# Optimization experiments

Hardware: AMD Instinct MI355X
Metric: run time of the kernel (lower is better)

Reference implementation:

```python
import jax, jax.numpy as jnp
import numpy as np
from itertools import product as iter_product

N_QUBITS = 6
DIM = 2 ** N_QUBITS            # 64
N_GEN = DIM * DIM - 1          # 4095
DEPTH = 4
N_OBS = 15

_GENS = None

def _build_generators(n):
    I = np.eye(2, dtype=np.complex64)
    X = np.array([[0, 1], [1, 0]], np.complex64)
    Y = np.array([[0, -1j], [1j, 0]], np.complex64)
    Z = np.array([[1, 0], [0, -1]], np.complex64)
    P = [I, X, Y, Z]
    gens = []
    for idx in iter_product(range(4), repeat=n):
        if all(i == 0 for i in idx):
            continue
        m = P[idx[0]]
        for k in range(1, n):
            m = np.kron(m, P[idx[k]])
        gens.append(m)
    return jnp.asarray(np.stack(gens))  # [4^n-1, 2^n, 2^n] complex64

def _gens():
    global _GENS
    if _GENS is None:
        _GENS = _build_generators(N_QUBITS)
    return _GENS

def _apply_ry(psi, q, theta, n):
    # psi: [B, 2^n] complex; RY(theta) on qubit q
    B = psi.shape[0]
    x = psi.reshape(B, 2 ** q, 2, 2 ** (n - q - 1))
    c = jnp.cos(theta / 2)
    s = jnp.sin(theta / 2)
    s0, s1 = x[:, :, 0, :], x[:, :, 1, :]
    x = jnp.stack([c * s0 - s * s1, s * s0 + c * s1], axis=2)
    return x.reshape(B, -1)

def _apply_cnot(psi, c, t, n):
    # psi: [B, 2^n]; CNOT control c, target t
    B = psi.shape[0]
    x = psi.reshape((B,) + (2,) * n)
    ax_c, ax_t = 1 + c, 1 + t
    x0 = jnp.take(x, 0, axis=ax_c)
    x1 = jnp.take(x, 1, axis=ax_c)
    ax_t2 = ax_t - (1 if ax_t > ax_c else 0)
    x1 = jnp.flip(x1, axis=ax_t2)
    x = jnp.stack([x0, x1], axis=ax_c)
    return x.reshape(B, -1)

def _make_hermitians(A, B, D):
    # create_Hermitian vectorized over the m observables.
    # h[i,j] = A[idx]+iB[idx] for j<i (row-major lower-tri), h[i-1,i-1]=D[i];
    # then H = h + h^H.
    il, jl = jnp.tril_indices(DIM, -1)  # row-major order matches count+j loop
    di = jnp.arange(DIM - 1)

    def one(a, b, d):
        h = jnp.zeros((DIM, DIM), jnp.complex64)
        h = h.at[il, jl].set(a + 1j * b)
        h = h.at[di, di].set(d[1:].astype(jnp.complex64))
        return h + h.conj().T

    return jax.vmap(one)(A, B, D)  # [m, DIM, DIM]

def setup_inputs() -> dict:
    key = jax.random.key(0)
    ks = jax.random.split(key, 8)
    batch, input_dim, hidden = 256, 1024, 2047
    n_off = DIM * (DIM - 1) // 2  # 2016
    return {
        "x": jax.random.normal(ks[0], (batch, input_dim), jnp.float32),
        "W1": 0.02 * jax.random.normal(ks[1], (input_dim, hidden), jnp.float32),
        "b1": jnp.zeros((hidden,), jnp.float32),
        "W2": 0.02 * jax.random.normal(ks[2], (hidden, N_GEN), jnp.float32),
        "b2": jnp.zeros((N_GEN,), jnp.float32),
        "var_params": 0.01 * jax.random.normal(ks[3], (DEPTH, N_QUBITS), jnp.float32),
        "A": 2.0 * jax.random.normal(ks[4], (N_OBS, n_off), jnp.float32),
        "B": 2.0 * jax.random.normal(ks[5], (N_OBS, n_off), jnp.float32),
        "D": 2.0 * jax.random.normal(ks[6], (N_OBS, DIM), jnp.float32),
    }

def reference(x, W1, b1, W2, b2, var_params, A, B, D):
    n = N_QUBITS
    # encoding projection: Linear -> SiLU -> Linear
    h = jax.nn.silu(x @ W1 + b1)
    theta = h @ W2 + b2  # [batch, 4^n - 1]
    gens = _gens()  # [n_gen, dim, dim] complex64 (constant)
    # A_mat = sum_g theta_g G_g (Hermitian), U = exp(i A_mat)
    Amat = jnp.einsum('bg,gij->bij', theta.astype(jnp.complex64), gens)
    U = jax.vmap(jax.scipy.linalg.expm)(1j * Amat)  # [batch, dim, dim]
    psi = U[:, :, 0]  # apply to |0...0>
    # hardware-efficient VQC: RY layer + CNOT ring per depth
    for d in range(DEPTH):
        for q in range(n):
            psi = _apply_ry(psi, q, var_params[d, q], n)
        for q in range(n):
            psi = _apply_cnot(psi, q, (q + 1) % n, n)
    H = _make_hermitians(A, B, D)  # [m, dim, dim]
    # expectation <psi|H_w|psi>
    exp = jnp.einsum('bi,wij,bj->bw', psi.conj(), H, psi).real
    return exp  # [batch, n_observables]
```

## Files before the change

### kernel.cpp

```cpp
#include <hip/hip_runtime.h>
#include <math.h>

typedef unsigned short ushort_t;
typedef __attribute__((ext_vector_type(8))) short bf16x8_t;
typedef __attribute__((ext_vector_type(4))) float f32x4_t;

__device__ __forceinline__ ushort_t f2bf(float x) {
  unsigned u = __float_as_uint(x);
  unsigned r = (u + 0x7fffu + ((u >> 16) & 1u)) >> 16;
  return (ushort_t)r;
}
__device__ __forceinline__ float bf2f(ushort_t h) {
  return __uint_as_float(((unsigned)h) << 16);
}
__device__ __forceinline__ void tsplit(float v, unsigned& h, unsigned& l) {
  unsigned u = __float_as_uint(v);
  h = u >> 16;
  float lo = v - __uint_as_float(u & 0xffff0000u);
  l = __float_as_uint(lo) >> 16;
}

__device__ __forceinline__ void transpose_tile(
    const float* __restrict__ W, ushort_t* __restrict__ Wh,
    ushort_t* __restrict__ Wl, int K, int N, int Kpad, int n0, int k0, int t) {
  __shared__ float sh[32][33];
  const int tx = t & 31, ty = t >> 5;
#pragma unroll
  for (int i = 0; i < 4; ++i) {
    int k = k0 + i * 8 + ty;
    float v = (k < K && (n0 + tx) < N) ? W[(size_t)k * N + n0 + tx] : 0.f;
    sh[tx][i * 8 + ty] = v;
  }
  __syncthreads();
#pragma unroll
  for (int i = 0; i < 4; ++i) {
    int n = n0 + i * 8 + ty;
    int kk = k0 + tx;
    float v = sh[i * 8 + ty][tx];
    size_t o = (size_t)n * Kpad + kk;
    unsigned h, l;
    tsplit(v, h, l);
    Wh[o] = (ushort_t)h;
    Wl[o] = (ushort_t)l;
  }
}

__global__ __launch_bounds__(256) void prep_kernel(
    const float* __restrict__ x, const float* __restrict__ W1,
    const float* __restrict__ W2,
    ushort_t* __restrict__ xh, ushort_t* __restrict__ xl,
    ushort_t* __restrict__ w1h, ushort_t* __restrict__ w1l,
    ushort_t* __restrict__ w2h, ushort_t* __restrict__ w2l) {
  const int bid = blockIdx.x;
  const int t = threadIdx.x;
  if (bid < 256) {
    int i4 = bid * 256 + t;
    float4 v = ((const float4*)x)[i4];
    unsigned h0, l0, h1, l1, h2, l2, h3, l3;
    tsplit(v.x, h0, l0); tsplit(v.y, h1, l1);
    tsplit(v.z, h2, l2); tsplit(v.w, h3, l3);
    uint2 ph, pl;
    ph.x = h0 | (h1 << 16); ph.y = h2 | (h3 << 16);
    pl.x = l0 | (l1 << 16); pl.y = l2 | (l3 << 16);
    ((uint2*)xh)[i4] = ph;
    ((uint2*)xl)[i4] = pl;
  } else if (bid < 256 + 2048) {
    int tau = bid - 256;
    transpose_tile(W1, w1h, w1l, 1024, 2047, 1024,
                   (tau & 63) * 32, (tau >> 6) * 32, t);
  } else {
    int tau = bid - 2304;
    transpose_tile(W2, w2h, w2l, 2047, 4095, 2048,
                   (tau & 127) * 32, (tau >> 7) * 32, t);
  }
}

#define LSTR 40
__global__ __launch_bounds__(256) void gemm_fused_kernel(
    const ushort_t* __restrict__ Ah, const ushort_t* __restrict__ Al,
    const ushort_t* __restrict__ Bh, const ushort_t* __restrict__ Bl,
    float* __restrict__ part, int KA, int KH, int Npad) {
  __shared__ ushort_t lds[4][64 * LSTR];
  const int t = threadIdx.x;
  const int lane = t & 63;
  const int wv = t >> 6;
  const int lane15 = lane & 15;
  const int quad = lane >> 4;
  const int wm = wv >> 1, wn = wv & 1;
  const int m0 = blockIdx.y * 64;
  const int n0 = blockIdx.x * 64;
  const int ks = blockIdx.z;

  const ushort_t* src = (wv == 0) ? Ah : (wv == 1) ? Al : (wv == 2) ? Bh : Bl;
  const int rowBase = (wv < 2) ? m0 : n0;
  ushort_t* dst = &lds[wv][0];

  f32x4_t acc[2][2];
#pragma unroll
  for (int i = 0; i < 2; ++i)
#pragma unroll
    for (int j = 0; j < 2; ++j) acc[i][j] = (f32x4_t){0.f, 0.f, 0.f, 0.f};

  const int iters = KH >> 5;
  const int kbase = ks * KH;
  for (int kt = 0; kt < iters; ++kt) {
    const int k0 = kbase + (kt << 5);
#pragma unroll
    for (int q = 0; q < 4; ++q) {
      int r = q * 16 + (lane >> 2);
      int c = (lane & 3) * 8;
      *(int4*)&dst[r * LSTR + c] =
          *(const int4*)(src + (size_t)(rowBase + r) * KA + k0 + c);
    }
    __syncthreads();
    bf16x8_t afh[2], afl[2], bfh[2], bfl[2];
#pragma unroll
    for (int i = 0; i < 2; ++i) {
      int mr = wm * 32 + i * 16 + lane15;
      afh[i] = *(const bf16x8_t*)&lds[0][mr * LSTR + quad * 8];
      afl[i] = *(const bf16x8_t*)&lds[1][mr * LSTR + quad * 8];
      int nr = wn * 32 + i * 16 + lane15;
      bfh[i] = *(const bf16x8_t*)&lds[2][nr * LSTR + quad * 8];
      bfl[i] = *(const bf16x8_t*)&lds[3][nr * LSTR + quad * 8];
    }
#pragma unroll
    for (int i = 0; i < 2; ++i)
#pragma unroll
      for (int j = 0; j < 2; ++j) {
        acc[i][j] = __builtin_amdgcn_mfma_f32_16x16x32_bf16(
            afh[i], bfh[j], acc[i][j], 0, 0, 0);
        acc[i][j] = __builtin_amdgcn_mfma_f32_16x16x32_bf16(
            afh[i], bfl[j], acc[i][j], 0, 0, 0);
        acc[i][j] = __builtin_amdgcn_mfma_f32_16x16x32_bf16(
            afl[i], bfh[j], acc[i][j], 0, 0, 0);
      }
    __syncthreads();
  }
  float* pbase = part + (size_t)ks * 256 * Npad;
#pragma unroll
  for (int i = 0; i < 2; ++i)
#pragma unroll
    for (int j = 0; j < 2; ++j) {
      int row0 = m0 + wm * 32 + i * 16 + quad * 4;
      int col = n0 + wn * 32 + j * 16 + lane15;
#pragma unroll
      for (int reg = 0; reg < 4; ++reg)
        pbase[(size_t)(row0 + reg) * Npad + col] = acc[i][j][reg];
    }
}

__global__ __launch_bounds__(256) void reduce1_kernel(
    const float* __restrict__ p, const float* __restrict__ b1,
    ushort_t* __restrict__ hh, ushort_t* __restrict__ hl) {
  int idx = blockIdx.x * 256 + threadIdx.x;
  int n = idx & 2047;
  float v = p[idx] + p[idx + 256 * 2048];
  if (n < 2047) {
    v += b1[n];
    v = v / (1.f + expf(-v));
  } else {
    v = 0.f;
  }
  unsigned h, l;
  tsplit(v, h, l);
  hh[idx] = (ushort_t)h;
  hl[idx] = (ushort_t)l;
}

#define TM 64
#define TN 64
#define TK 16
__global__ __launch_bounds__(256) void gemm_tiled(
    const float* __restrict__ X, const float* __restrict__ W,
    const float* __restrict__ bias, float* __restrict__ out,
    int M, int N, int K, int ldx, int ldw, int ldo, int doSilu, int padN)
{
  __shared__ float Xs[TK][TM + 4];
  __shared__ float Ws[TK][TN + 4];
  const int t = threadIdx.x;
  const int n0 = blockIdx.x * TN;
  const int m0 = blockIdx.y * TM;
  const int tr = t >> 4, tc = t & 15;
  float acc[4][4];
#pragma unroll
  for (int i = 0; i < 4; ++i)
#pragma unroll
    for (int j = 0; j < 4; ++j) acc[i][j] = 0.f;
  const int xr = t >> 2, xk = (t & 3) * 4;
  const int wk = t >> 4, wc = (t & 15) * 4;
  for (int k0 = 0; k0 < K; k0 += TK) {
    {
      const float* xp = X + (size_t)(m0 + xr) * ldx + (k0 + xk);
      float xv[4];
      if (k0 + xk + 3 < K) {
        float4 v = *(const float4*)xp;
        xv[0] = v.x; xv[1] = v.y; xv[2] = v.z; xv[3] = v.w;
      } else {
#pragma unroll
        for (int e = 0; e < 4; ++e) xv[e] = (k0 + xk + e < K) ? xp[e] : 0.f;
      }
#pragma unroll
      for (int e = 0; e < 4; ++e) Xs[xk + e][xr] = xv[e];
    }
    {
      const int kk = k0 + wk;
      const float* wp = W + (size_t)kk * ldw + (n0 + wc);
      const bool kv = kk < K;
#pragma unroll
      for (int e = 0; e < 4; ++e) {
        int n = n0 + wc + e;
        Ws[wk][wc + e] = (kv && n < N) ? wp[e] : 0.f;
      }
    }
    __syncthreads();
#pragma unroll
    for (int k = 0; k < TK; ++k) {
      float4 av = *(const float4*)&Xs[k][tr * 4];
      float4 bv = *(const float4*)&Ws[k][tc * 4];
      float a4[4] = {av.x, av.y, av.z, av.w};
      float b4[4] = {bv.x, bv.y, bv.z, bv.w};
#pragma unroll
      for (int i = 0; i < 4; ++i)
#pragma unroll
        for (int j = 0; j < 4; ++j)
          acc[i][j] = fmaf(a4[i], b4[j], acc[i][j]);
    }
    __syncthreads();
  }
#pragma unroll
  for (int i = 0; i < 4; ++i) {
    const int mrow = m0 + tr * 4 + i;
    float* op = out + (size_t)mrow * ldo;
#pragma unroll
    for (int j = 0; j < 4; ++j) {
      const int n = n0 + tc * 4 + j;
      if (n < N) {
        float v = acc[i][j] + bias[n];
        if (doSilu) v = v / (1.f + expf(-v));
        op[n] = v;
      } else if (n < padN) {
        op[n] = 0.f;
      }
    }
  }
}

#define RS 72
#define PL (64 * RS)

__device__ __forceinline__ void qmm4(
    const ushort_t* __restrict__ Prm, const ushort_t* __restrict__ Qcm,
    float* ore, float* oim, int mt, int nt, int quad, int l15)
{
  f32x4_t aR = (f32x4_t){0.f, 0.f, 0.f, 0.f};
  f32x4_t aN = (f32x4_t){0.f, 0.f, 0.f, 0.f};
  f32x4_t aI = (f32x4_t){0.f, 0.f, 0.f, 0.f};
#pragma unroll
  for (int kb = 0; kb < 2; ++kb) {
    const int ko = kb * 32 + quad * 8;
    const int ra = (mt * 16 + l15) * RS + ko;
    bf16x8_t arh = *(const bf16x8_t*)&Prm[0 * PL + ra];
    bf16x8_t arl = *(const bf16x8_t*)&Prm[1 * PL + ra];
    bf16x8_t aih = *(const bf16x8_t*)&Prm[2 * PL + ra];
    bf16x8_t ail = *(const bf16x8_t*)&Prm[3 * PL + ra];
    const int rb = (nt * 16 + l15) * RS + ko;
    bf16x8_t brh = *(const bf16x8_t*)&Qcm[0 * PL + rb];
    bf16x8_t brl = *(const bf16x8_t*)&Qcm[1 * PL + rb];
    bf16x8_t bih = *(const bf16x8_t*)&Qcm[2 * PL + rb];
    bf16x8_t bil = *(const bf16x8_t*)&Qcm[3 * PL + rb];
    aR = __builtin_amdgcn_mfma_f32_16x16x32_bf16(arh, brh, aR, 0, 0, 0);
    aR = __builtin_amdgcn_mfma_f32_16x16x32_bf16(arh, brl, aR, 0, 0, 0);
    aR = __builtin_amdgcn_mfma_f32_16x16x32_bf16(arl, brh, aR, 0, 0, 0);
    aN = __builtin_amdgcn_mfma_f32_16x16x32_bf16(aih, bih, aN, 0, 0, 0);
    aN = __builtin_amdgcn_mfma_f32_16x16x32_bf16(aih, bil, aN, 0, 0, 0);
    aN = __builtin_amdgcn_mfma_f32_16x16x32_bf16(ail, bih, aN, 0, 0, 0);
    aI = __builtin_amdgcn_mfma_f32_16x16x32_bf16(arh, bih, aI, 0, 0, 0);
    aI = __builtin_amdgcn_mfma_f32_16x16x32_bf16(arh, bil, aI, 0, 0, 0);
    aI = __builtin_amdgcn_mfma_f32_16x16x32_bf16(arl, bih, aI, 0, 0, 0);
    aI = __builtin_amdgcn_mfma_f32_16x16x32_bf16(aih, brh, aI, 0, 0, 0);
    aI = __builtin_amdgcn_mfma_f32_16x16x32_bf16(aih, brl, aI, 0, 0, 0);
    aI = __builtin_amdgcn_mfma_f32_16x16x32_bf16(ail, brh, aI, 0, 0, 0);
  }
#pragma unroll
  for (int rg = 0; rg < 4; ++rg) {
    ore[rg] = aR[rg] - aN[rg];
    oim[rg] = aI[rg];
  }
}

__device__ __forceinline__ void stage_rm4(
    ushort_t* rm, const float* re, const float* im, int mt, int nt,
    int quad, int l15)
{
  unsigned rh[4], rl[4], ih[4], il[4];
#pragma unroll
  for (int rg = 0; rg < 4; ++rg) {
    tsplit(re[rg], rh[rg], rl[rg]);
    tsplit(im[rg], ih[rg], il[rg]);
  }
#pragma unroll
  for (int rg = 0; rg < 4; ++rg) {
    int idx = (mt * 16 + quad * 4 + rg) * RS + nt * 16 + l15;
    rm[0 * PL + idx] = (ushort_t)rh[rg];
    rm[1 * PL + idx] = (ushort_t)rl[rg];
    rm[2 * PL + idx] = (ushort_t)ih[rg];
    rm[3 * PL + idx] = (ushort_t)il[rg];
  }
}

__device__ __forceinline__ void stage_cm4(
    ushort_t* cm, const float* re, const float* im, int mt, int nt,
    int quad, int l15)
{
  unsigned rh[4], rl[4], ih[4], il[4];
#pragma unroll
  for (int rg = 0; rg < 4; ++rg) {
    tsplit(re[rg], rh[rg], rl[rg]);
    tsplit(im[rg], ih[rg], il[rg]);
  }
  int base = (nt * 16 + l15) * RS + mt * 16 + quad * 4;
  uint2 p;
  p.x = rh[0] | (rh[1] << 16); p.y = rh[2] | (rh[3] << 16);
  *(uint2*)&cm[0 * PL + base] = p;
  p.x = rl[0] | (rl[1] << 16); p.y = rl[2] | (rl[3] << 16);
  *(uint2*)&cm[1 * PL + base] = p;
  p.x = ih[0] | (ih[1] << 16); p.y = ih[2] | (ih[3] << 16);
  *(uint2*)&cm[2 * PL + base] = p;
  p.x = il[0] | (il[1] << 16); p.y = il[2] | (il[3] << 16);
  *(uint2*)&cm[3 * PL + base] = p;
}

__device__ __forceinline__ void stage_both4(
    ushort_t* rm, ushort_t* cm, const float* re, const float* im,
    int mt, int nt, int quad, int l15)
{
  stage_rm4(rm, re, im, mt, nt, quad, l15);
  stage_cm4(cm, re, im, mt, nt, quad, l15);
}

__global__ __launch_bounds__(1024, 4) void quantum_kernel(
    const float* __restrict__ pin,
    const float* __restrict__ b2g,
    const float* __restrict__ vp,
    const float* __restrict__ Aobs,
    const float* __restrict__ Bobs,
    const float* __restrict__ Dobs,
    float* __restrict__ out,
    int fused)
{
  __shared__ __align__(16) ushort_t PQ[2][8 * PL];
  __shared__ float ps[128];
  __shared__ float scr16[16];
  __shared__ float csb[24], snb[24];
  __shared__ float sAf;
  __shared__ int   sS;

  float*  thetas = (float*)&PQ[1][0];
  float2* Als    = (float2*)&PQ[0][0];

  const int t = threadIdx.x;
  const int b = blockIdx.x;
  const int lane = t & 63;
  const int w = t >> 6;
  const int quad = lane >> 4;
  const int l15 = lane & 15;
  const int mt = w >> 2, nt = w & 3;

  float ssq;
  {
    float4 v = ((const float4*)(pin + (size_t)b * 4096))[t];
    if (fused) {
#pragma unroll
      for (int k = 1; k < 4; ++k) {
        float4 u =
            ((const float4*)(pin + (size_t)k * 256 * 4096 + (size_t)b * 4096))[t];
        v.x += u.x; v.y += u.y; v.z += u.z; v.w += u.w;
      }
      int n0i = 4 * t;
      v.x += b2g[n0i];
      v.y += b2g[n0i + 1];
      v.z += b2g[n0i + 2];
      if (n0i + 3 < 4095) v.w += b2g[n0i + 3];
    }
    if (t == 1023) v.w = 0.f;
    thetas[4 * t + 0] = v.x; thetas[4 * t + 1] = v.y;
    thetas[4 * t + 2] = v.z; thetas[4 * t + 3] = v.w;
    ssq = v.x * v.x + v.y * v.y + v.z * v.z + v.w * v.w;
  }
#pragma unroll
  for (int mm = 1; mm < 64; mm <<= 1) ssq += __shfl_xor(ssq, mm);
  if (lane == 0) scr16[w] = ssq;
  __syncthreads();
  if (w == 0) {
    float s = (lane < 16) ? scr16[lane] : 0.f;
#pragma unroll
    for (int mm = 1; mm < 64; mm <<= 1) s += __shfl_xor(s, mm);
    if (lane == 0) {
      float frob = fmaxf(8.f * sqrtf(s), 1e-3f);
      sAf = frob;
      float bound = 0.30f * frob;
      int sc = (bound > 1.f) ? (int)ceilf(log2f(bound)) : 0;
      sS = sc < 0 ? 0 : (sc > 12 ? 12 : sc);
    }
  } else if (w == 1 && lane < 24) {
    float sn, cs;
    sincosf(vp[lane] * 0.5f, &sn, &cs);
    snb[lane] = sn;
    csb[lane] = cs;
  }
  __syncthreads();
  const int sPow = sS;

  for (int xx = 0; xx < 4; ++xx) {
    const int x = w + 16 * xx;
    const int z = lane;
    int g1 = 0;
#pragma unroll
    for (int bq = 0; bq < 6; ++bq) {
      int xb = (x >> bq) & 1, zb = (z >> bq) & 1;
      int dig = xb ? (zb ? 2 : 1) : (zb ? 3 : 0);
      g1 |= dig << (2 * bq);
    }
    float tv = (g1 == 0) ? 0.f : thetas[g1 - 1];
    int pc = __popc(x & z) & 3;
    float re, im;
    switch (pc) {
      case 0:  re = tv;  im = 0.f;  break;
      case 1:  re = 0.f; im = -tv;  break;
      case 2:  re = -tv; im = 0.f;  break;
      default: re = 0.f; im = tv;   break;
    }
#pragma unroll
    for (int mk = 1; mk < 64; mk <<= 1) {
      float ore = __shfl_xor(re, mk);
      float oim = __shfl_xor(im, mk);
      if (z & mk) { re = ore - re; im = oim - im; }
      else        { re = re + ore; im = im + oim; }
    }
    Als[z * 66 + (z ^ x)] = make_float2(re, im);
  }
  __syncthreads();

  const float scl = ldexpf(1.f, -sPow);
  float bre[4], bim[4];
#pragma unroll
  for (int rg = 0; rg < 4; ++rg) {
    int row = mt * 16 + quad * 4 + rg;
    int col = nt * 16 + l15;
    float2 v = Als[row * 66 + col];
    bre[rg] = -v.y * scl;
    bim[rg] =  v.x * scl;
  }
  __syncthreads();

  ushort_t* b0 = &PQ[0][0];
  ushort_t* b1 = &PQ[1][0];
  stage_both4(b0, b0 + 4 * PL, bre, bim, mt, nt, quad, l15);
  __syncthreads();
  float b2re[4], b2im[4];
  qmm4(b0, b0 + 4 * PL, b2re, b2im, mt, nt, quad, l15);
  stage_both4(b1, b1 + 4 * PL, b2re, b2im, mt, nt, quad, l15);
  __syncthreads();
  float b3re[4], b3im[4];
  qmm4(b1, b0 + 4 * PL, b3re, b3im, mt, nt, quad, l15);

  const float c3 = 1.f / 6.f, c4 = 1.f / 24.f, c5 = 1.f / 120.f;
  const float c6 = 1.f / 720.f, c7 = 1.f / 5040.f, c8 = 1.f / 40320.f;
  float s1re[4], s1im[4], p0re[4], p0im[4];
#pragma unroll
  for (int rg = 0; rg < 4; ++rg) {
    float dg = (mt == nt && l15 == quad * 4 + rg) ? 1.f : 0.f;
    s1re[rg] = c4 * dg + c5 * bre[rg] + c6 * b2re[rg] + c7 * b3re[rg];
    s1im[rg] =           c5 * bim[rg] + c6 * b2im[rg] + c7 * b3im[rg];
    p0re[rg] = dg + bre[rg] + 0.5f * b2re[rg] + c3 * b3re[rg];
    p0im[rg] =      bim[rg] + 0.5f * b2im[rg] + c3 * b3im[rg];
  }
  float b4re[4], b4im[4];
  qmm4(b1, b1 + 4 * PL, b4re, b4im, mt, nt, quad, l15);
#pragma unroll
  for (int rg = 0; rg < 4; ++rg) {
    s1re[rg] += c8 * b4re[rg];
    s1im[rg] += c8 * b4im[rg];
  }
  __syncthreads();
  stage_rm4(b0, s1re, s1im, mt, nt, quad, l15);
  stage_cm4(b0 + 4 * PL, b4re, b4im, mt, nt, quad, l15);
  __syncthreads();
  float ure[4], uim[4];
  qmm4(b0, b0 + 4 * PL, ure, uim, mt, nt, quad, l15);
#pragma unroll
  for (int rg = 0; rg < 4; ++rg) {
    ure[rg] += p0re[rg];
    uim[rg] += p0im[rg];
  }

  int cur = 1;
  for (int q = 0; q < sPow; ++q) {
    ushort_t* bb = &PQ[cur][0];
    stage_both4(bb, bb + 4 * PL, ure, uim, mt, nt, quad, l15);
    __syncthreads();
    qmm4(bb, bb + 4 * PL, ure, uim, mt, nt, quad, l15);
    cur ^= 1;
  }

  if (nt == 0 && l15 == 0) {
#pragma unroll
    for (int rg = 0; rg < 4; ++rg) {
      int row = mt * 16 + quad * 4 + rg;
      ps[2 * row] = ure[rg];
      ps[2 * row + 1] = uim[rg];
    }
  }
  __syncthreads();

  if (t < 64) {
    float pre = ps[2 * t], pim = ps[2 * t + 1];
#pragma unroll
    for (int d = 0; d < 4; ++d) {
#pragma unroll
      for (int q = 0; q < 6; ++q) {
        float s = snb[d * 6 + q], c = csb[d * 6 + q];
        int bpos = 5 - q;
        int bit = (t >> bpos) & 1;
        float ore = __shfl_xor(pre, 1 << bpos);
        float oim = __shfl_xor(pim, 1 << bpos);
        float sg = bit ? s : -s;
        pre = c * pre + sg * ore;
        pim = c * pim + sg * oim;
      }
#pragma unroll
      for (int q = 0; q < 6; ++q) {
        int bc = 5 - q;
        int bt = 5 - ((q + 1) % 6);
        float ore = __shfl_xor(pre, 1 << bt);
        float oim = __shfl_xor(pim, 1 << bt);
        int ctrl = (t >> bc) & 1;
        pre = ctrl ? ore : pre;
        pim = ctrl ? oim : pim;
      }
    }
    ps[2 * t] = pre; ps[2 * t + 1] = pim;
  }
  __syncthreads();

  float* Rt = (float*)&PQ[0][0];
  float* It = Rt + 2016;
  for (int p = t; p < 2016; p += 1024) {
    int i = (int)((1.f + sqrtf(8.f * (float)p + 1.f)) * 0.5f);
    while (i * (i - 1) / 2 > p) --i;
    while (i * (i + 1) / 2 <= p) ++i;
    int j = p - i * (i - 1) / 2;
    float pri = ps[2 * i], pii = ps[2 * i + 1];
    float prj = ps[2 * j], pij = ps[2 * j + 1];
    Rt[p] = pri * prj + pii * pij;
    It[p] = pri * pij - pii * prj;
  }
  __syncthreads();

  if (w < 15) {
    float xr = ps[2 * lane], xi = ps[2 * lane + 1];
    float mypsq = xr * xr + xi * xi;
    const float* Ap = Aobs + w * 2016;
    const float* Bp = Bobs + w * 2016;
    float part = 0.f;
    for (int p2 = lane; p2 < 1008; p2 += 64) {
      float2 a = *(const float2*)&Ap[2 * p2];
      float2 bb2 = *(const float2*)&Bp[2 * p2];
      float2 rt = *(const float2*)&Rt[2 * p2];
      float2 it = *(const float2*)&It[2 * p2];
      part += a.x * rt.x - bb2.x * it.x;
      part += a.y * rt.y - bb2.y * it.y;
    }
    if (lane < 63) part += Dobs[w * 64 + lane + 1] * mypsq;
#pragma unroll
    for (int mm = 1; mm < 64; mm <<= 1) part += __shfl_xor(part, mm);
    if (lane == 0) out[b * 15 + w] = 2.f * part;
  }
}

extern "C" void kernel_launch(void* const* d_in, const int* in_sizes, int n_in,
                              void* d_out, int out_size, void* d_ws, size_t ws_size,
                              hipStream_t stream) {
  const float* x  = (const float*)d_in[0];
  const float* W1 = (const float*)d_in[1];
  const float* b1 = (const float*)d_in[2];
  const float* W2 = (const float*)d_in[3];
  const float* b2 = (const float*)d_in[4];
  const float* vp = (const float*)d_in[5];
  const float* Ao = (const float*)d_in[6];
  const float* Bo = (const float*)d_in[7];
  const float* Do = (const float*)d_in[8];
  float* out = (float*)d_out;

  const size_t O_XH  = 0;
  const size_t O_XL  = 524288;
  const size_t O_W1H = 1048576;
  const size_t O_W1L = 5242880;
  const size_t O_PG1 = 9437184;
  const size_t O_PT  = 0;
  const size_t O_W2H = 16777216;
  const size_t O_W2L = 33554432;
  const size_t O_HH  = 50331648;
  const size_t O_HL  = 51380224;
  const size_t NEED  = 52428800;

  if (ws_size >= NEED) {
    char* ws = (char*)d_ws;
    ushort_t* xh  = (ushort_t*)(ws + O_XH);
    ushort_t* xl  = (ushort_t*)(ws + O_XL);
    ushort_t* w1h = (ushort_t*)(ws + O_W1H);
    ushort_t* w1l = (ushort_t*)(ws + O_W1L);
    float* partg1 = (float*)(ws + O_PG1);
    float* part16 = (float*)(ws + O_PT);
    ushort_t* w2h = (ushort_t*)(ws + O_W2H);
    ushort_t* w2l = (ushort_t*)(ws + O_W2L);
    ushort_t* hh  = (ushort_t*)(ws + O_HH);
    ushort_t* hl  = (ushort_t*)(ws + O_HL);

    prep_kernel<<<10496, 256, 0, stream>>>(x, W1, W2, xh, xl, w1h, w1l, w2h, w2l);
    gemm_fused_kernel<<<dim3(32, 4, 2), 256, 0, stream>>>(
        xh, xl, w1h, w1l, partg1, 1024, 512, 2048);
    reduce1_kernel<<<2048, 256, 0, stream>>>(partg1, b1, hh, hl);
    gemm_fused_kernel<<<dim3(64, 4, 4), 256, 0, stream>>>(
        hh, hl, w2h, w2l, part16, 2048, 512, 4096);
    quantum_kernel<<<256, 1024, 0, stream>>>(part16, b2, vp, Ao, Bo, Do, out, 1);
  } else {
    float* h     = (float*)d_ws;
    float* theta = h + 256 * 2048;
    gemm_tiled<<<dim3(32, 4), 256, 0, stream>>>(
        x, W1, b1, h, 256, 2047, 1024, 1024, 2047, 2048, 1, 2048);
    gemm_tiled<<<dim3(64, 4), 256, 0, stream>>>(
        h, W2, b2, theta, 256, 4095, 2047, 2048, 4095, 4096, 0, 4096);
    quantum_kernel<<<256, 1024, 0, stream>>>(theta, b2, vp, Ao, Bo, Do, out, 0);
  }
}
```

Before: 177.8 us.

## Add 128x64-tile GEMM for second projection and vectorize transpose stores

Replaces the generic split-K GEMM used for the second projection with a specialized kernel that uses 128x64 output tiles, 4 waves each computing 64x32, and warp-specialized loads where two waves fill the A hi/lo tiles and two fill the B hi/lo tiles. The larger M tile halves the number of B-tile reloads and increases MFMA work per shared-memory load. It also vectorizes the bf16 hi/lo stores in the weight transpose to 8-byte writes per thread. In exchange the launch has half as many blocks and needs more accumulator registers, and the load work per wave is unbalanced.

```diff
diff --git a/kernel.cpp b/kernel.cpp
--- a/kernel.cpp
+++ b/kernel.cpp
@@ -5,14 +5,6 @@
 typedef __attribute__((ext_vector_type(8))) short bf16x8_t;
 typedef __attribute__((ext_vector_type(4))) float f32x4_t;
 
-__device__ __forceinline__ ushort_t f2bf(float x) {
-  unsigned u = __float_as_uint(x);
-  unsigned r = (u + 0x7fffu + ((u >> 16) & 1u)) >> 16;
-  return (ushort_t)r;
-}
-__device__ __forceinline__ float bf2f(ushort_t h) {
-  return __uint_as_float(((unsigned)h) << 16);
-}
 __device__ __forceinline__ void tsplit(float v, unsigned& h, unsigned& l) {
   unsigned u = __float_as_uint(v);
   h = u >> 16;
@@ -32,17 +24,17 @@
     sh[tx][i * 8 + ty] = v;
   }
   __syncthreads();
-#pragma unroll
-  for (int i = 0; i < 4; ++i) {
-    int n = n0 + i * 8 + ty;
-    int kk = k0 + tx;
-    float v = sh[i * 8 + ty][tx];
-    size_t o = (size_t)n * Kpad + kk;
-    unsigned h, l;
-    tsplit(v, h, l);
-    Wh[o] = (ushort_t)h;
-    Wl[o] = (ushort_t)l;
-  }
+  const int nn = t >> 3;
+  const int kq = t & 7;
+  unsigned h[4], l[4];
+#pragma unroll
+  for (int e = 0; e < 4; ++e) tsplit(sh[nn][kq * 4 + e], h[e], l[e]);
+  size_t o = (size_t)(n0 + nn) * Kpad + k0 + kq * 4;
+  uint2 ph, pl;
+  ph.x = h[0] | (h[1] << 16); ph.y = h[2] | (h[3] << 16);
+  pl.x = l[0] | (l[1] << 16); pl.y = l[2] | (l[3] << 16);
+  *(uint2*)&Wh[o] = ph;
+  *(uint2*)&Wl[o] = pl;
 }
 
 __global__ __launch_bounds__(256) void prep_kernel(
@@ -149,6 +141,89 @@
     }
 }
 
+__global__ __launch_bounds__(256) void gemm2k_kernel(
+    const ushort_t* __restrict__ Ah, const ushort_t* __restrict__ Al,
+    const ushort_t* __restrict__ Bh, const ushort_t* __restrict__ Bl,
+    float* __restrict__ part) {
+  __shared__ ushort_t Ab[2][128 * LSTR];
+  __shared__ ushort_t Bb[2][64 * LSTR];
+  const int t = threadIdx.x;
+  const int lane = t & 63;
+  const int wv = t >> 6;
+  const int l15 = lane & 15;
+  const int quad = lane >> 4;
+  const int wm = wv >> 1, wn = wv & 1;
+  const int m0 = blockIdx.y * 128;
+  const int n0 = blockIdx.x * 64;
+  const int ks = blockIdx.z;
+
+  f32x4_t acc[4][2];
+#pragma unroll
+  for (int i = 0; i < 4; ++i)
+#pragma unroll
+    for (int j = 0; j < 2; ++j) acc[i][j] = (f32x4_t){0.f, 0.f, 0.f, 0.f};
+
+  for (int kt = 0; kt < 16; ++kt) {
+    const int k0 = ks * 512 + kt * 32;
+    if (wv < 2) {
+      const ushort_t* src = wv ? Al : Ah;
+      ushort_t* dst = Ab[wv];
+#pragma unroll
+      for (int q = 0; q < 8; ++q) {
+        int r = q * 16 + (lane >> 2);
+        int c = (lane & 3) * 8;
+        *(int4*)&dst[r * LSTR + c] =
+            *(const int4*)(src + (size_t)(m0 + r) * 2048 + k0 + c);
+      }
+    } else {
+      const ushort_t* src = (wv == 3) ? Bl : Bh;
+      ushort_t* dst = Bb[wv - 2];
+#pragma unroll
+      for (int q = 0; q < 4; ++q) {
+        int r = q * 16 + (lane >> 2);
+        int c = (lane & 3) * 8;
+        *(int4*)&dst[r * LSTR + c] =
+            *(const int4*)(src + (size_t)(n0 + r) * 2048 + k0 + c);
+      }
+    }
+    __syncthreads();
+    bf16x8_t bfh[2], bfl[2];
+#pragma unroll
+    for (int j = 0; j < 2; ++j) {
+      int nr = wn * 32 + j * 16 + l15;
+      bfh[j] = *(const bf16x8_t*)&Bb[0][nr * LSTR + quad * 8];
+      bfl[j] = *(const bf16x8_t*)&Bb[1][nr * LSTR + quad * 8];
+    }
+#pragma unroll
+    for (int i = 0; i < 4; ++i) {
+      int mr = wm * 64 + i * 16 + l15;
+      bf16x8_t afh = *(const bf16x8_t*)&Ab[0][mr * LSTR + quad * 8];
+      bf16x8_t afl = *(const bf16x8_t*)&Ab[1][mr * LSTR + quad * 8];
+#pragma unroll
+      for (int j = 0; j < 2; ++j) {
+        acc[i][j] = __builtin_amdgcn_mfma_f32_16x16x32_bf16(
+            afh, bfh[j], acc[i][j], 0, 0, 0);
+        acc[i][j] = __builtin_amdgcn_mfma_f32_16x16x32_bf16(
+            afh, bfl[j], acc[i][j], 0, 0, 0);
+        acc[i][j] = __builtin_amdgcn_mfma_f32_16x16x32_bf16(
+            afl, bfh[j], acc[i][j], 0, 0, 0);
+      }
+    }
+    __syncthreads();
+  }
+  float* pbase = part + (size_t)ks * 256 * 4096;
+#pragma unroll
+  for (int i = 0; i < 4; ++i)
+#pragma unroll
+    for (int j = 0; j < 2; ++j) {
+      int row0 = m0 + wm * 64 + i * 16 + quad * 4;
+      int col = n0 + wn * 32 + j * 16 + l15;
+#pragma unroll
+      for (int rg = 0; rg < 4; ++rg)
+        pbase[(size_t)(row0 + rg) * 4096 + col] = acc[i][j][rg];
+    }
+}
+
 __global__ __launch_bounds__(256) void reduce1_kernel(
     const float* __restrict__ p, const float* __restrict__ b1,
     ushort_t* __restrict__ hh, ushort_t* __restrict__ hl) {
@@ -621,8 +696,7 @@
     gemm_fused_kernel<<<dim3(32, 4, 2), 256, 0, stream>>>(
         xh, xl, w1h, w1l, partg1, 1024, 512, 2048);
     reduce1_kernel<<<2048, 256, 0, stream>>>(partg1, b1, hh, hl);
-    gemm_fused_kernel<<<dim3(64, 4, 4), 256, 0, stream>>>(
-        hh, hl, w2h, w2l, part16, 2048, 512, 4096);
+    gemm2k_kernel<<<dim3(64, 2, 4), 256, 0, stream>>>(hh, hl, w2h, w2l, part16);
     quantum_kernel<<<256, 1024, 0, stream>>>(part16, b2, vp, Ao, Bo, Do, out, 1);
   } else {
     float* h     = (float*)d_ws;
```

Measured after the change: 181.3 us. No clear change (+1.9%).
